# Kernel optimization log

Hardware: AMD Instinct MI355X
Metric: run time of the kernel (lower is better)

## Reference

```python
import jax, jax.numpy as jnp
import numpy as np

# physical constants from init_kwargs
N_ACT = 10.0                      # adaptive_activation_n (same for all layers)
MU1, MU2 = 1.0, 10.0
SIGMA = 24.5
G = 0.98
RHO1, RHO2 = 100.0, 1000.0
U_REF, L_REF = 1.0, 0.5
RHO_REF = RHO2
EPS = 2.220446049250313e-16       # np.finfo(float).eps used in abs_interface_grad
ONE_WE = SIGMA / (RHO_REF * U_REF ** 2 * L_REF)
ONE_FR = G * L_REF / U_REF ** 2
RE_DEN = RHO_REF * U_REF * L_REF


def setup_inputs() -> dict:
    key = jax.random.key(0)
    ks = jax.random.split(key, 8)
    N, H, NL = 32768, 250, 7

    def glorot(k, shape):
        fan_in, fan_out = shape[-2], shape[-1]
        s = jnp.sqrt(2.0 / (fan_in + fan_out)).astype(jnp.float32)
        return jax.random.normal(k, shape, dtype=jnp.float32) * s

    return {
        "x": jax.random.normal(ks[0], (N, 1), dtype=jnp.float32),
        "y": jax.random.normal(ks[1], (N, 1), dtype=jnp.float32),
        "t": jax.random.uniform(ks[2], (N, 1), dtype=jnp.float32),
        "W_in": glorot(ks[3], (3, H)),
        "b_in": jnp.zeros((H,), jnp.float32),
        "W_h": glorot(ks[4], (NL - 1, H, H)),
        "b_h": jnp.zeros((NL - 1, H), jnp.float32),
        "W_out": glorot(ks[5], (H, 4)),   # 4 heads: u, v, p, a
        "b_out": jnp.zeros((4,), jnp.float32),
        "act_coeff": jnp.full((NL,), 0.1, jnp.float32),  # adaptive activation coeffs
    }


def _mlp(pt, W_in, b_in, W_h, b_h, W_out, b_out, act_coeff):
    # pt: (3,) -> (4,) outputs [u, v, p=exp(z), a=sigmoid(z)]
    h = jnp.tanh(N_ACT * act_coeff[0] * (pt @ W_in + b_in))
    for i in range(W_h.shape[0]):  # structural loop over 6 hidden layers
        h = jnp.tanh(N_ACT * act_coeff[i + 1] * (h @ W_h[i] + b_h[i]))
    z = h @ W_out + b_out
    return jnp.stack([z[0], z[1], jnp.exp(z[2]), jax.nn.sigmoid(z[3])])


def _pde_residuals(x, y, t, W_in, b_in, W_h, b_h, W_out, b_out, act_coeff):
    pts = jnp.concatenate([x, y, t], axis=1)  # (N, 3)
    f = lambda p: _mlp(p, W_in, b_in, W_h, b_h, W_out, b_out, act_coeff)
    vals = jax.vmap(f)(pts)                              # (N, 4)
    jac = jax.vmap(jax.jacfwd(f))(pts)                   # (N, 4, 3)
    hess = jax.vmap(jax.jacfwd(jax.jacfwd(f)))(pts)      # (N, 4, 3, 3)

    u, v, a = vals[:, 0], vals[:, 1], vals[:, 3]
    u_x, u_y, u_t = jac[:, 0, 0], jac[:, 0, 1], jac[:, 0, 2]
    v_x, v_y, v_t = jac[:, 1, 0], jac[:, 1, 1], jac[:, 1, 2]
    p_x, p_y = jac[:, 2, 0], jac[:, 2, 1]
    a_x, a_y, a_t = jac[:, 3, 0], jac[:, 3, 1], jac[:, 3, 2]
    u_xx, u_yy = hess[:, 0, 0, 0], hess[:, 0, 1, 1]
    v_xx, v_yy = hess[:, 1, 0, 0], hess[:, 1, 1, 1]
    a_xx, a_yy, a_xy = hess[:, 3, 0, 0], hess[:, 3, 1, 1], hess[:, 3, 0, 1]

    mu = MU2 + (MU1 - MU2) * a
    mu_x = (MU1 - MU2) * a_x
    mu_y = (MU1 - MU2) * a_y
    rho = RHO2 + (RHO1 - RHO2) * a

    g = jnp.sqrt(a_x ** 2 + a_y ** 2 + EPS)
    curvature = -((a_xx + a_yy) / g
                  - (a_x ** 2 * a_xx + a_y ** 2 * a_yy + 2.0 * a_x * a_y * a_xy) / (g ** 3))

    one_Re = mu / RE_DEN
    one_Re_x = mu_x / RE_DEN
    one_Re_y = mu_y / RE_DEN

    PDE_m = u_x + v_y
    PDE_a = a_t + u * a_x + v * a_y
    PDE_u = ((u_t + u * u_x + v * u_y) * rho / RHO_REF + p_x
             - ONE_WE * curvature * a_x - one_Re * (u_xx + u_yy)
             - 2.0 * one_Re_x * u_x - one_Re_y * (u_y + v_x))
    PDE_v = ((v_t + u * v_x + v * v_y) * rho / RHO_REF + p_y
             - ONE_WE * curvature * a_y - one_Re * (v_xx + v_yy)
             - rho / RHO_REF * ONE_FR
             - 2.0 * one_Re_y * v_y - one_Re_x * (u_y + v_x))
    return jnp.stack([PDE_m, PDE_u, PDE_v, PDE_a], axis=1)  # (N, 4)


def reference(x, y, t, W_in, b_in, W_h, b_h, W_out, b_out, act_coeff):
    r = _pde_residuals(x, y, t, W_in, b_in, W_h, b_h, W_out, b_out, act_coeff)
    # match PDE_caller's tuple of (N,1) residuals
    return (r[:, 0:1], r[:, 1:2], r[:, 2:3], r[:, 3:4])
```

## Files before the change

kernel.cpp:

```cpp
#include <hip/hip_runtime.h>
#include <math.h>
#include <stdint.h>

#define HP 256
#define PTS 16
#define ROWS 128
#define PSTR 264
#define NLAYER 6
#define WT_ELEMS (6*256*256)

typedef _Float16 half8 __attribute__((ext_vector_type(8)));
typedef float  float16v __attribute__((ext_vector_type(16)));

#define C_WI 0
#define C_BI 768
#define C_BH 1024
#define C_WO 2560
#define C_TOT 3584

__device__ __forceinline__ float fast_tanh(float x) {
    float e = __expf(2.0f * x);
    return 1.0f - __fdividef(2.0f, e + 1.0f);
}

__device__ __forceinline__ float16v zero16() {
    float16v z;
    #pragma unroll
    for (int i = 0; i < 16; ++i) z[i] = 0.0f;
    return z;
}

__device__ __forceinline__ int arow(int P, int c) {
    return 32*(P >> 2) + 16*((P >> 1) & 1) + 4*(P & 1) + 8*(c >> 2) + (c & 3);
}

#define MFMA16(A,B,Cc) __builtin_amdgcn_mfma_f32_32x32x16_f16((A),(B),(Cc),0,0,0)

__global__ void prep_kernel(const float* __restrict__ W_in, const float* __restrict__ b_in,
                            const float* __restrict__ W_h,  const float* __restrict__ b_h,
                            const float* __restrict__ W_out, void* __restrict__ wsv)
{
    _Float16* wt = (_Float16*)wsv;
    float* cf = (float*)((char*)wsv + (size_t)WT_ELEMS * 2);

    int i0 = blockIdx.x * blockDim.x + threadIdx.x;
    int stride = gridDim.x * blockDim.x;
    for (int i = i0; i < WT_ELEMS; i += stride) {
        int j    = i & 7;
        int lane = (i >> 3) & 63;
        int st   = (i >> 9) & 7;
        int s    = (i >> 12) & 15;
        int L    = i >> 16;
        int lo5 = lane & 31, hi5 = lane >> 5;
        int n = 32*st + lo5;
        int k = 16*s + 8*hi5 + j;
        wt[i] = (_Float16)((n < 250 && k < 250) ? W_h[(L*250 + k)*250 + n] : 0.0f);
    }
    for (int i = i0; i < C_TOT; i += stride) {
        float v = 0.0f;
        if (i < C_BI) { int r = i >> 8, j = i & 255; if (j < 250) v = W_in[r*250 + j]; }
        else if (i < C_BH) { int j = i - C_BI; if (j < 250) v = b_in[j]; }
        else if (i < C_WO) { int idx = i - C_BH; int l = idx >> 8, j = idx & 255; if (j < 250) v = b_h[l*250 + j]; }
        else { int idx = i - C_WO; int k = idx >> 2, o = idx & 3; if (k < 250) v = W_out[k*4 + o]; }
        cf[i] = v;
    }
}

__launch_bounds__(512, 4)
__global__ void pinn_mfma(const float* __restrict__ xg, const float* __restrict__ yg,
                          const float* __restrict__ tg, const void* __restrict__ wsv,
                          const float* __restrict__ b_out, const float* __restrict__ act,
                          float* __restrict__ out, int N)
{
    __shared__ _Float16 Ah[ROWS * PSTR];
    __shared__ float zo[PTS][28];

    const _Float16* __restrict__ wt = (const _Float16*)wsv;
    const float* __restrict__ cf = (const float*)((const char*)wsv + (size_t)WT_ELEMS * 2);

    const int tid  = threadIdx.x;
    const int lane = tid & 63;
    const int w    = tid >> 6;
    const int lo5  = lane & 31;
    const int hi5  = lane >> 5;
    const int n0   = 32*w + lo5;

    {
        int j   = tid & 255;
        int hf  = tid >> 8;
        float wi0 = cf[C_WI + j], wi1 = cf[C_WI + 256 + j], wi2 = cf[C_WI + 512 + j];
        float biv = cf[C_BI + j];
        float c0 = 10.0f * act[0];
        #pragma unroll
        for (int p8 = 0; p8 < 8; ++p8) {
            int p  = 8*hf + p8;
            int gp = blockIdx.x * PTS + p;
            gp = gp < N ? gp : N - 1;
            float px = xg[gp], py = yg[gp], pt = tg[gp];
            float z = px*wi0 + py*wi1 + pt*wi2 + biv;
            float y = fast_tanh(c0 * z);
            float s = 1.0f - y*y;
            float cs = c0 * s;
            float m2 = -2.0f * c0 * cs * y;
            float o[8];
            o[0] = y;           o[1] = cs*wi0;      o[2] = cs*wi1;      o[3] = cs*wi2;
            o[4] = m2*wi0*wi0;  o[5] = m2*wi1*wi1;  o[6] = m2*wi0*wi1;  o[7] = 0.0f;
            #pragma unroll
            for (int c = 0; c < 8; ++c)
                Ah[arow(p, c)*PSTR + j] = (_Float16)o[c];
        }
    }

    for (int L = 0; L < NLAYER; ++L) {
        float cc = 10.0f * act[L + 1];
        const _Float16* __restrict__ ph = wt + ((size_t)L << 16) + ((size_t)w << 9)
                                             + (size_t)lane * 8;

        half8 Bq[4];
        #pragma unroll
        for (int i = 0; i < 4; ++i)
            Bq[i] = *(const half8*)(ph + 4096*i);

        float16v m[4];
        #pragma unroll
        for (int rt = 0; rt < 4; ++rt) m[rt] = zero16();

        __syncthreads();

        const int abase = lo5 * PSTR + 8*hi5;
        half8 a0[4], a1[4];
        #pragma unroll
        for (int rt = 0; rt < 4; ++rt) {
            a0[rt] = *(const half8*)&Ah[abase + 32*rt*PSTR];
            a1[rt] = *(const half8*)&Ah[abase + 32*rt*PSTR + 16];
        }

        #pragma unroll
        for (int s = 0; s < 16; ++s) {
            half8 b = Bq[s & 3];
            if (s < 12)
                Bq[s & 3] = *(const half8*)(ph + 4096*(s + 4));
            half8 cur[4];
            #pragma unroll
            for (int rt = 0; rt < 4; ++rt) { cur[rt] = a0[rt]; a0[rt] = a1[rt]; }
            if (s < 14) {
                #pragma unroll
                for (int rt = 0; rt < 4; ++rt)
                    a1[rt] = *(const half8*)&Ah[abase + 32*rt*PSTR + 16*(s + 2)];
            }
            #pragma unroll
            for (int rt = 0; rt < 4; ++rt)
                m[rt] = MFMA16(cur[rt], b, m[rt]);
        }

        __syncthreads();

        float bb = cf[C_BH + (L << 8) + n0];

        #pragma unroll
        for (int rt = 0; rt < 4; ++rt) {
            float16v mv = m[rt];
            #pragma unroll
            for (int pp = 0; pp < 2; ++pp) {
                float z   = mv[8*pp+0] + bb;
                float zx  = mv[8*pp+1];
                float zy  = mv[8*pp+2];
                float zt  = mv[8*pp+3];
                float zxx = mv[8*pp+4];
                float zyy = mv[8*pp+5];
                float zxy = mv[8*pp+6];
                float y   = fast_tanh(cc * z);
                float sh  = 1.0f - y*y;
                float cs  = cc * sh;
                float m2c = -2.0f * cc * cs * y;
                int r0 = (32*rt + 16*pp + 4*hi5) * PSTR + n0;
                Ah[r0 + 0*PSTR] = (_Float16)y;
                Ah[r0 + 1*PSTR] = (_Float16)(cs*zx);
                Ah[r0 + 2*PSTR] = (_Float16)(cs*zy);
                Ah[r0 + 3*PSTR] = (_Float16)(cs*zt);
                int r1 = r0 + 8*PSTR;
                Ah[r1 + 0*PSTR] = (_Float16)(cs*zxx + m2c*zx*zx);
                Ah[r1 + 1*PSTR] = (_Float16)(cs*zyy + m2c*zy*zy);
                Ah[r1 + 2*PSTR] = (_Float16)(cs*zxy + m2c*zx*zy);
                Ah[r1 + 3*PSTR] = (_Float16)0.0f;
            }
        }
    }

    __syncthreads();
    if (tid < PTS * 28) {
        int p = tid / 28, idx = tid % 28;
        int c = idx >> 2, o = idx & 3;
        const _Float16* rh = &Ah[arow(p, c) * PSTR];
        float s = 0.0f;
        for (int k = 0; k < HP; ++k)
            s += (float)rh[k] * cf[C_WO + 4*k + o];
        zo[p][idx] = s;
    }
    __syncthreads();

    if (tid < PTS) {
        int gp = blockIdx.x * PTS + tid;
        if (gp < N) {
            float zc[7][4];
            #pragma unroll
            for (int c = 0; c < 7; ++c)
                #pragma unroll
                for (int o = 0; o < 4; ++o)
                    zc[c][o] = zo[tid][c*4 + o] + (c == 0 ? b_out[o] : 0.0f);

            float u  = zc[0][0], vv = zc[0][1];
            float u_x = zc[1][0], u_y = zc[2][0], u_t = zc[3][0];
            float u_xx = zc[4][0], u_yy = zc[5][0];
            float v_x = zc[1][1], v_y = zc[2][1], v_t = zc[3][1];
            float v_xx = zc[4][1], v_yy = zc[5][1];

            float ep  = expf(zc[0][2]);
            float p_x = ep * zc[1][2], p_y = ep * zc[2][2];

            float a   = 1.0f / (1.0f + expf(-zc[0][3]));
            float sp  = a * (1.0f - a);
            float spp = sp * (1.0f - 2.0f*a);
            float z1a = zc[1][3], z2a = zc[2][3];
            float a_x = sp * z1a, a_y = sp * z2a, a_t = sp * zc[3][3];
            float a_xx = spp*z1a*z1a + sp*zc[4][3];
            float a_yy = spp*z2a*z2a + sp*zc[5][3];
            float a_xy = spp*z1a*z2a + sp*zc[6][3];

            float mu_x = -9.0f*a_x, mu_y = -9.0f*a_y;
            float mu   = 10.0f - 9.0f*a;
            float rr   = 1.0f - 0.9f*a;
            float g  = sqrtf(a_x*a_x + a_y*a_y + 2.220446049250313e-16f);
            float g3 = g*g*g;
            float curv = -((a_xx + a_yy)/g
                         - (a_x*a_x*a_xx + a_y*a_y*a_yy + 2.0f*a_x*a_y*a_xy)/g3);
            float one_Re   = mu   * 0.002f;
            float one_Re_x = mu_x * 0.002f;
            float one_Re_y = mu_y * 0.002f;

            float PDE_m = u_x + v_y;
            float PDE_a = a_t + u*a_x + vv*a_y;
            float PDE_u = (u_t + u*u_x + vv*u_y)*rr + p_x - 0.049f*curv*a_x
                        - one_Re*(u_xx + u_yy) - 2.0f*one_Re_x*u_x - one_Re_y*(u_y + v_x);
            float PDE_v = (v_t + u*v_x + vv*v_y)*rr + p_y - 0.049f*curv*a_y
                        - one_Re*(v_xx + v_yy) - rr*0.49f
                        - 2.0f*one_Re_y*v_y - one_Re_x*(u_y + v_x);

            out[0*N + gp] = PDE_m;
            out[1*N + gp] = PDE_u;
            out[2*N + gp] = PDE_v;
            out[3*N + gp] = PDE_a;
        }
    }
}

extern "C" void kernel_launch(void* const* d_in, const int* in_sizes, int n_in,
                              void* d_out, int out_size, void* d_ws, size_t ws_size,
                              hipStream_t stream)
{
    const float* x     = (const float*)d_in[0];
    const float* y     = (const float*)d_in[1];
    const float* t     = (const float*)d_in[2];
    const float* W_in  = (const float*)d_in[3];
    const float* b_in  = (const float*)d_in[4];
    const float* W_h   = (const float*)d_in[5];
    const float* b_h   = (const float*)d_in[6];
    const float* W_out = (const float*)d_in[7];
    const float* b_out = (const float*)d_in[8];
    const float* act   = (const float*)d_in[9];
    float* out = (float*)d_out;
    int N = in_sizes[0];

    hipLaunchKernelGGL(prep_kernel, dim3(512), dim3(256), 0, stream,
                       W_in, b_in, W_h, b_h, W_out, d_ws);
    int nb = (N + PTS - 1) / PTS;
    hipLaunchKernelGGL(pinn_mfma, dim3(nb), dim3(512), 0, stream,
                       x, y, t, d_ws, b_out, act, out, N);
}
```

Before: 313.7 us.

## Retile hidden-layer MFMA as 2x2 warp grid and vectorize output-head LDS reads

Each of the 8 warps now computes a 64-row by 64-column block (2 row tiles times 2 column tiles) instead of 128 rows by 32 columns. This halves the LDS A-fragment reads per warp. Each warp loads two B streams from global memory, so global weight traffic per warp doubles while per-block weight traffic is unchanged. The output-head dot product also reads activations as half8 vectors instead of scalar halfs. Register pressure stays about the same: four accumulators plus two B queues.

```diff
diff --git a/kernel.cpp b/kernel.cpp
--- a/kernel.cpp
+++ b/kernel.cpp
@@ -81,9 +81,10 @@
     const int tid  = threadIdx.x;
     const int lane = tid & 63;
     const int w    = tid >> 6;
+    const int rg   = w >> 2;
+    const int csp  = w & 3;
     const int lo5  = lane & 31;
     const int hi5  = lane >> 5;
-    const int n0   = 32*w + lo5;
 
     {
         int j   = tid & 255;
@@ -113,76 +114,81 @@
 
     for (int L = 0; L < NLAYER; ++L) {
         float cc = 10.0f * act[L + 1];
-        const _Float16* __restrict__ ph = wt + ((size_t)L << 16) + ((size_t)w << 9)
-                                             + (size_t)lane * 8;
-
-        half8 Bq[4];
-        #pragma unroll
-        for (int i = 0; i < 4; ++i)
-            Bq[i] = *(const half8*)(ph + 4096*i);
-
-        float16v m[4];
-        #pragma unroll
-        for (int rt = 0; rt < 4; ++rt) m[rt] = zero16();
+        const _Float16* __restrict__ ph0 = wt + ((size_t)L << 16) + ((size_t)(2*csp) << 9)
+                                              + (size_t)lane * 8;
+        const _Float16* __restrict__ ph1 = ph0 + 512;
+
+        half8 B0q[4], B1q[4];
+        #pragma unroll
+        for (int i = 0; i < 4; ++i) {
+            B0q[i] = *(const half8*)(ph0 + 4096*i);
+            B1q[i] = *(const half8*)(ph1 + 4096*i);
+        }
+
+        float16v m00 = zero16(), m01 = zero16(), m10 = zero16(), m11 = zero16();
 
         __syncthreads();
 
-        const int abase = lo5 * PSTR + 8*hi5;
-        half8 a0[4], a1[4];
-        #pragma unroll
-        for (int rt = 0; rt < 4; ++rt) {
-            a0[rt] = *(const half8*)&Ah[abase + 32*rt*PSTR];
-            a1[rt] = *(const half8*)&Ah[abase + 32*rt*PSTR + 16];
-        }
+        const int abase = (64*rg + lo5) * PSTR + 8*hi5;
+        half8 a0q[2], a1q[2];
+        a0q[0] = *(const half8*)&Ah[abase];
+        a0q[1] = *(const half8*)&Ah[abase + 16];
+        a1q[0] = *(const half8*)&Ah[abase + 32*PSTR];
+        a1q[1] = *(const half8*)&Ah[abase + 32*PSTR + 16];
 
         #pragma unroll
         for (int s = 0; s < 16; ++s) {
-            half8 b = Bq[s & 3];
-            if (s < 12)
-                Bq[s & 3] = *(const half8*)(ph + 4096*(s + 4));
-            half8 cur[4];
-            #pragma unroll
-            for (int rt = 0; rt < 4; ++rt) { cur[rt] = a0[rt]; a0[rt] = a1[rt]; }
+            half8 b0 = B0q[s & 3];
+            half8 b1 = B1q[s & 3];
+            half8 a0 = a0q[s & 1];
+            half8 a1 = a1q[s & 1];
+            if (s < 12) {
+                B0q[s & 3] = *(const half8*)(ph0 + 4096*(s + 4));
+                B1q[s & 3] = *(const half8*)(ph1 + 4096*(s + 4));
+            }
             if (s < 14) {
+                a0q[s & 1] = *(const half8*)&Ah[abase + 16*(s + 2)];
+                a1q[s & 1] = *(const half8*)&Ah[abase + 32*PSTR + 16*(s + 2)];
+            }
+            m00 = MFMA16(a0, b0, m00);
+            m01 = MFMA16(a0, b1, m01);
+            m10 = MFMA16(a1, b0, m10);
+            m11 = MFMA16(a1, b1, m11);
+        }
+
+        __syncthreads();
+
+        #pragma unroll
+        for (int c = 0; c < 2; ++c) {
+            int ncol = 64*csp + 32*c + lo5;
+            float bb = cf[C_BH + (L << 8) + ncol];
+            #pragma unroll
+            for (int t = 0; t < 2; ++t) {
+                float16v mv = t ? (c ? m11 : m10) : (c ? m01 : m00);
                 #pragma unroll
-                for (int rt = 0; rt < 4; ++rt)
-                    a1[rt] = *(const half8*)&Ah[abase + 32*rt*PSTR + 16*(s + 2)];
-            }
-            #pragma unroll
-            for (int rt = 0; rt < 4; ++rt)
-                m[rt] = MFMA16(cur[rt], b, m[rt]);
-        }
-
-        __syncthreads();
-
-        float bb = cf[C_BH + (L << 8) + n0];
-
-        #pragma unroll
-        for (int rt = 0; rt < 4; ++rt) {
-            float16v mv = m[rt];
-            #pragma unroll
-            for (int pp = 0; pp < 2; ++pp) {
-                float z   = mv[8*pp+0] + bb;
-                float zx  = mv[8*pp+1];
-                float zy  = mv[8*pp+2];
-                float zt  = mv[8*pp+3];
-                float zxx = mv[8*pp+4];
-                float zyy = mv[8*pp+5];
-                float zxy = mv[8*pp+6];
-                float y   = fast_tanh(cc * z);
-                float sh  = 1.0f - y*y;
-                float cs  = cc * sh;
-                float m2c = -2.0f * cc * cs * y;
-                int r0 = (32*rt + 16*pp + 4*hi5) * PSTR + n0;
-                Ah[r0 + 0*PSTR] = (_Float16)y;
-                Ah[r0 + 1*PSTR] = (_Float16)(cs*zx);
-                Ah[r0 + 2*PSTR] = (_Float16)(cs*zy);
-                Ah[r0 + 3*PSTR] = (_Float16)(cs*zt);
-                int r1 = r0 + 8*PSTR;
-                Ah[r1 + 0*PSTR] = (_Float16)(cs*zxx + m2c*zx*zx);
-                Ah[r1 + 1*PSTR] = (_Float16)(cs*zyy + m2c*zy*zy);
-                Ah[r1 + 2*PSTR] = (_Float16)(cs*zxy + m2c*zx*zy);
-                Ah[r1 + 3*PSTR] = (_Float16)0.0f;
+                for (int pp = 0; pp < 2; ++pp) {
+                    float z   = mv[8*pp+0] + bb;
+                    float zx  = mv[8*pp+1];
+                    float zy  = mv[8*pp+2];
+                    float zt  = mv[8*pp+3];
+                    float zxx = mv[8*pp+4];
+                    float zyy = mv[8*pp+5];
+                    float zxy = mv[8*pp+6];
+                    float y   = fast_tanh(cc * z);
+                    float sh  = 1.0f - y*y;
+                    float cs  = cc * sh;
+                    float m2c = -2.0f * cc * cs * y;
+                    int r0 = (64*rg + 32*t + 16*pp + 4*hi5) * PSTR + ncol;
+                    Ah[r0 + 0*PSTR] = (_Float16)y;
+                    Ah[r0 + 1*PSTR] = (_Float16)(cs*zx);
+                    Ah[r0 + 2*PSTR] = (_Float16)(cs*zy);
+                    Ah[r0 + 3*PSTR] = (_Float16)(cs*zt);
+                    int r1 = r0 + 8*PSTR;
+                    Ah[r1 + 0*PSTR] = (_Float16)(cs*zxx + m2c*zx*zx);
+                    Ah[r1 + 1*PSTR] = (_Float16)(cs*zyy + m2c*zy*zy);
+                    Ah[r1 + 2*PSTR] = (_Float16)(cs*zxy + m2c*zx*zy);
+                    Ah[r1 + 3*PSTR] = (_Float16)0.0f;
+                }
             }
         }
     }
@@ -193,8 +199,12 @@
         int c = idx >> 2, o = idx & 3;
         const _Float16* rh = &Ah[arow(p, c) * PSTR];
         float s = 0.0f;
-        for (int k = 0; k < HP; ++k)
-            s += (float)rh[k] * cf[C_WO + 4*k + o];
+        for (int kq = 0; kq < HP/8; ++kq) {
+            half8 h = *(const half8*)(rh + 8*kq);
+            #pragma unroll
+            for (int j = 0; j < 8; ++j)
+                s += (float)h[j] * cf[C_WO + 4*(8*kq + j) + o];
+        }
         zo[p][idx] = s;
     }
     __syncthreads();
```

New measurement: 316.1 us. About the same (+0.8%).
